# Kernel tuning notes

Measured on AMD Instinct MI355X. Metric: run time of the kernel, lower is better.

Reference implementation:

```python
import jax, jax.numpy as jnp
import numpy as np

PAD_LEFT, PAD_RIGHT = 2, 3


def setup_inputs() -> dict:
    key = jax.random.key(0)
    ks = jax.random.split(key, 7)
    B, T, I, H, O = 256, 2048, 32, 64, 16
    s_ih = 1.0 / np.sqrt(H)
    return {
        "x": jax.random.normal(ks[0], (B, T, I), dtype=jnp.float32),
        "W_ih": jax.random.uniform(ks[1], (H, I), jnp.float32, -s_ih, s_ih),
        "W_hh": jax.random.uniform(ks[2], (H, H), jnp.float32, -s_ih, s_ih),
        "b_ih": jax.random.uniform(ks[3], (H,), jnp.float32, -s_ih, s_ih),
        "b_hh": jax.random.uniform(ks[4], (H,), jnp.float32, -s_ih, s_ih),
        "W_fc": jax.random.uniform(ks[5], (O, H), jnp.float32, -s_ih, s_ih),
        "b_fc": jax.random.uniform(ks[6], (O,), jnp.float32, -s_ih, s_ih),
    }


def reference(x, W_ih, W_hh, b_ih, b_hh, W_fc, b_fc):
    # x: (B, T, I). Zero-pad time axis (ZeroPad1d on permuted tensor).
    B, T, I = x.shape
    H = W_ih.shape[0]
    x_p = jnp.pad(x, ((0, 0), (PAD_LEFT, PAD_RIGHT), (0, 0)))  # (B, Tp, I)
    Tp = T + PAD_LEFT + PAD_RIGHT

    # Precompute input projections for all steps: (Tp, B, H)
    xin = jnp.einsum('bti,hi->tbh', x_p, W_ih) + b_ih + b_hh

    def step(carry, xt):
        h, acc = carry
        h_new = jnp.tanh(xt + h @ W_hh.T)
        return (h_new, acc + h_new), None

    h0 = jnp.zeros((B, H), dtype=x.dtype)
    (h_last, h_sum), _ = jax.lax.scan(step, (h0, jnp.zeros((B, H), x.dtype)), xin)

    # Dropout3d is identity in eval mode; mean over padded time, then fc + relu.
    aggregated = h_sum / Tp  # (B, H)
    return jax.nn.relu(aggregated @ W_fc.T + b_fc)
```

## Files before the change

### kernel.cpp

```cpp
#include <hip/hip_runtime.h>

constexpr int kB = 256;
constexpr int kT = 2048;
constexpr int kI = 32;
constexpr int kH = 64;
constexpr int kO = 16;
constexpr int kPadL = 2;
constexpr int kPadR = 3;
constexpr int kTp = kT + kPadL + kPadR;
constexpr int kCT = 64;
constexpr int kNC = kT / kCT;

constexpr float kS = 1.4426950408889634f;

constexpr unsigned kRbufOff  = 0;
constexpr unsigned kXinOff   = 128;
constexpr unsigned kXinBytes = kCT * kH * 4;
constexpr unsigned kAggOff   = kXinOff + 2 * kXinBytes;
constexpr unsigned kSmemBytes = kAggOff + kH * 4;

typedef float    v2f __attribute__((ext_vector_type(2)));
typedef _Float16 v2h __attribute__((ext_vector_type(2)));
typedef unsigned v4u __attribute__((ext_vector_type(4)));

extern __shared__ char smem[];

__device__ __forceinline__ void pk_fma(v2f& d, v2f a, v2f b) {
  asm("v_pk_fma_f32 %0, %1, %2, %0" : "+v"(d) : "v"(a), "v"(b));
}

__device__ __forceinline__ v2h as_h2(unsigned u) {
  return __builtin_bit_cast(v2h, u);
}

__device__ __forceinline__ float dot2(v2h a, v2h b, float c) {
#if __has_builtin(__builtin_amdgcn_fdot2)
  return __builtin_amdgcn_fdot2(a, b, c, false);
#else
  return fmaf((float)a.x, (float)b.x, fmaf((float)a.y, (float)b.y, c));
#endif
}

__device__ __forceinline__ float exp2_fast(float x) {
#if __has_builtin(__builtin_amdgcn_exp2f)
  return __builtin_amdgcn_exp2f(x);
#else
  return exp2f(x);
#endif
}

#define STEP_LDS_MAIN(q0, q1, q2, q3, q4, q5, q6, q7, xn, rv, xaddr)  \
  asm volatile(                                                       \
      "ds_write_b16 %9, %10\n\t"                                      \
      "ds_read_b128 %0, %11 offset:0\n\t"                             \
      "ds_read_b128 %1, %11 offset:16\n\t"                            \
      "ds_read_b128 %2, %11 offset:32\n\t"                            \
      "ds_read_b128 %3, %11 offset:48\n\t"                            \
      "ds_read_b128 %4, %11 offset:64\n\t"                            \
      "ds_read_b128 %5, %11 offset:80\n\t"                            \
      "ds_read_b128 %6, %11 offset:96\n\t"                            \
      "ds_read_b128 %7, %11 offset:112\n\t"                           \
      "ds_read_b32 %8, %12\n\t"                                       \
      "s_waitcnt lgkmcnt(0)"                                          \
      : "=v"(q0), "=v"(q1), "=v"(q2), "=v"(q3),                       \
        "=v"(q4), "=v"(q5), "=v"(q6), "=v"(q7), "=v"(xn)              \
      : "v"(raddr), "v"(rv), "v"(rbase), "v"(xaddr))

#define STEP_LDS_NOX(q0, q1, q2, q3, q4, q5, q6, q7, rv)              \
  asm volatile(                                                       \
      "ds_write_b16 %8, %9\n\t"                                       \
      "ds_read_b128 %0, %10 offset:0\n\t"                             \
      "ds_read_b128 %1, %10 offset:16\n\t"                            \
      "ds_read_b128 %2, %10 offset:32\n\t"                            \
      "ds_read_b128 %3, %10 offset:48\n\t"                            \
      "ds_read_b128 %4, %10 offset:64\n\t"                            \
      "ds_read_b128 %5, %10 offset:80\n\t"                            \
      "ds_read_b128 %6, %10 offset:96\n\t"                            \
      "ds_read_b128 %7, %10 offset:112\n\t"                           \
      "s_waitcnt lgkmcnt(0)"                                          \
      : "=v"(q0), "=v"(q1), "=v"(q2), "=v"(q3),                       \
        "=v"(q4), "=v"(q5), "=v"(q6), "=v"(q7)                        \
      : "v"(raddr), "v"(rv), "v"(rbase))

__global__ __launch_bounds__(128) void rnn_fused(
    const float* __restrict__ x,
    const float* __restrict__ W_ih,
    const float* __restrict__ W_hh,
    const float* __restrict__ b_ih,
    const float* __restrict__ b_hh,
    const float* __restrict__ W_fc,
    const float* __restrict__ b_fc,
    float* __restrict__ out)
{
  const int b = blockIdx.x;
  const int lane = threadIdx.x & 63;
  const int wave = threadIdx.x >> 6;

  float rowsum = 0.0f;
#pragma unroll
  for (int j = 0; j < kH; j += 4) {
    float4 v = *(const float4*)(W_hh + lane * kH + j);
    rowsum += (v.x + v.y) + (v.z + v.w);
  }
  const float bias2 = 2.0f * kS * (b_ih[lane] + b_hh[lane] + rowsum);

  if (wave == 1) {
    v2f wi2[kI / 2];
#pragma unroll
    for (int i = 0; i < kI; i += 4) {
      float4 v = *(const float4*)(W_ih + lane * kI + i);
      wi2[i / 2 + 0] = v2f{2.0f * kS * v.x, 2.0f * kS * v.y};
      wi2[i / 2 + 1] = v2f{2.0f * kS * v.z, 2.0f * kS * v.w};
    }
    const float* xb = x + (size_t)b * kT * kI;

    auto fill = [&](int c, int buf) {
      const float* src = xb + (size_t)c * kCT * kI;
      float* dst = (float*)(smem + kXinOff + buf * kXinBytes);
#pragma unroll 2
      for (int t = 0; t < kCT; ++t) {
        const float4* row = (const float4*)(src + t * kI);
        v2f a0 = v2f{0.0f, 0.0f}, a1 = v2f{0.0f, 0.0f};
#pragma unroll
        for (int i2 = 0; i2 < 8; ++i2) {
          float4 v = row[i2];
          pk_fma(a0, wi2[2 * i2 + 0], v2f{v.x, v.y});
          pk_fma(a1, wi2[2 * i2 + 1], v2f{v.z, v.w});
        }
        dst[t * kH + lane] = bias2 + ((a0.x + a0.y) + (a1.x + a1.y));
      }
    };

    fill(0, 0);
    __syncthreads();
    for (int c = 0; c < kNC; ++c) {
      if (c + 1 < kNC) fill(c + 1, (c + 1) & 1);
      __syncthreads();
    }
    return;
  }

  v2h wh[kH / 2];
#pragma unroll
  for (int j = 0; j < kH; j += 2) {
    float w0 = W_hh[lane * kH + j + 0];
    float w1 = W_hh[lane * kH + j + 1];
    wh[j / 2] = v2h{(_Float16)(-4.0f * kS * w0), (_Float16)(-4.0f * kS * w1)};
  }

  const unsigned raddr = kRbufOff + (unsigned)lane * 2u;
  unsigned rbase = kRbufOff;

  float rsum = 0.0f;
  unsigned rv = (unsigned)__builtin_bit_cast(unsigned short, (_Float16)0.5f);

  auto tail = [&](const v4u& A, const v4u& B, const v4u& C, const v4u& D,
                  const v4u& E, const v4u& F, const v4u& G, const v4u& H,
                  float za_init) -> float {
    float za = za_init, zb = 0.0f, zc = 0.0f, zd = 0.0f;
    za = dot2(as_h2(A.x), wh[0], za);
    zb = dot2(as_h2(A.y), wh[1], zb);
    zc = dot2(as_h2(A.z), wh[2], zc);
    zd = dot2(as_h2(A.w), wh[3], zd);
    za = dot2(as_h2(B.x), wh[4], za);
    zb = dot2(as_h2(B.y), wh[5], zb);
    zc = dot2(as_h2(B.z), wh[6], zc);
    zd = dot2(as_h2(B.w), wh[7], zd);
    za = dot2(as_h2(C.x), wh[8], za);
    zb = dot2(as_h2(C.y), wh[9], zb);
    zc = dot2(as_h2(C.z), wh[10], zc);
    zd = dot2(as_h2(C.w), wh[11], zd);
    za = dot2(as_h2(D.x), wh[12], za);
    zb = dot2(as_h2(D.y), wh[13], zb);
    zc = dot2(as_h2(D.z), wh[14], zc);
    zd = dot2(as_h2(D.w), wh[15], zd);
    za = dot2(as_h2(E.x), wh[16], za);
    zb = dot2(as_h2(E.y), wh[17], zb);
    zc = dot2(as_h2(E.z), wh[18], zc);
    zd = dot2(as_h2(E.w), wh[19], zd);
    za = dot2(as_h2(F.x), wh[20], za);
    zb = dot2(as_h2(F.y), wh[21], zb);
    zc = dot2(as_h2(F.z), wh[22], zc);
    zd = dot2(as_h2(F.w), wh[23], zd);
    za = dot2(as_h2(G.x), wh[24], za);
    zb = dot2(as_h2(G.y), wh[25], zb);
    zc = dot2(as_h2(G.z), wh[26], zc);
    zd = dot2(as_h2(G.w), wh[27], zd);
    za = dot2(as_h2(H.x), wh[28], za);
    zb = dot2(as_h2(H.y), wh[29], zb);
    zc = dot2(as_h2(H.z), wh[30], zc);
    zd = dot2(as_h2(H.w), wh[31], zd);
    float z2 = (za + zb) + (zc + zd);
    float t = exp2_fast(z2);
    return __builtin_amdgcn_rcpf(1.0f + t);
  };

  auto pad_step = [&]() {
    v4u q0, q1, q2, q3, q4, q5, q6, q7;
    STEP_LDS_NOX(q0, q1, q2, q3, q4, q5, q6, q7, rv);
    float r = tail(q0, q1, q2, q3, q4, q5, q6, q7, bias2);
    rsum += r;
    rv = (unsigned)__builtin_bit_cast(unsigned short, (_Float16)r);
  };

  pad_step();
  pad_step();
  __syncthreads();

  for (int c = 0; c < kNC; ++c) {
    const unsigned xbase = kXinOff + (unsigned)(c & 1) * kXinBytes +
                           (unsigned)lane * 4u;
    float xc;
    asm volatile("ds_read_b32 %0, %1\n\ts_waitcnt lgkmcnt(0)"
                 : "=v"(xc) : "v"(xbase));
#pragma unroll 9
    for (int t = 0; t < kCT - 1; ++t) {
      v4u q0, q1, q2, q3, q4, q5, q6, q7;
      float xn;
      const unsigned xaddr = xbase + (unsigned)(t + 1) * (kH * 4u);
      STEP_LDS_MAIN(q0, q1, q2, q3, q4, q5, q6, q7, xn, rv, xaddr);
      float r = tail(q0, q1, q2, q3, q4, q5, q6, q7, xc);
      rsum += r;
      rv = (unsigned)__builtin_bit_cast(unsigned short, (_Float16)r);
      xc = xn;
    }
    {
      v4u q0, q1, q2, q3, q4, q5, q6, q7;
      STEP_LDS_NOX(q0, q1, q2, q3, q4, q5, q6, q7, rv);
      float r = tail(q0, q1, q2, q3, q4, q5, q6, q7, xc);
      rsum += r;
      rv = (unsigned)__builtin_bit_cast(unsigned short, (_Float16)r);
    }
    __syncthreads();
  }

  pad_step();
  pad_step();
  pad_step();

  float* aggbuf = (float*)(smem + kAggOff);
  aggbuf[lane] = 1.0f - 2.0f * rsum * (1.0f / (float)kTp);
  if (lane < kO) {
    float acc = b_fc[lane];
    const float* wf = W_fc + lane * kH;
#pragma unroll
    for (int j = 0; j < kH; ++j)
      acc = fmaf(wf[j], aggbuf[j], acc);
    out[b * kO + lane] = fmaxf(acc, 0.0f);
  }
}

extern "C" void kernel_launch(void* const* d_in, const int* in_sizes, int n_in,
                              void* d_out, int out_size, void* d_ws, size_t ws_size,
                              hipStream_t stream) {
  const float* x    = (const float*)d_in[0];
  const float* W_ih = (const float*)d_in[1];
  const float* W_hh = (const float*)d_in[2];
  const float* b_ih = (const float*)d_in[3];
  const float* b_hh = (const float*)d_in[4];
  const float* W_fc = (const float*)d_in[5];
  const float* b_fc = (const float*)d_in[6];
  float* out = (float*)d_out;

  rnn_fused<<<dim3(kB), dim3(128), kSmemBytes, stream>>>(
      x, W_ih, W_hh, b_ih, b_hh, W_fc, b_fc, out);
}
```

Before: 572.0 us.

## Interleave two batch recurrences per wave to hide LDS latency

```diff
diff --git a/kernel.cpp b/kernel.cpp
--- a/kernel.cpp
+++ b/kernel.cpp
@@ -8,16 +8,18 @@
 constexpr int kPadL = 2;
 constexpr int kPadR = 3;
 constexpr int kTp = kT + kPadL + kPadR;
-constexpr int kCT = 64;
+constexpr int kCT = 32;
 constexpr int kNC = kT / kCT;
 
 constexpr float kS = 1.4426950408889634f;
 
-constexpr unsigned kRbufOff  = 0;
-constexpr unsigned kXinOff   = 128;
+constexpr unsigned kRbufA = 0;
+constexpr unsigned kRbufB = 128;
+constexpr unsigned kXinA  = 256;
 constexpr unsigned kXinBytes = kCT * kH * 4;
-constexpr unsigned kAggOff   = kXinOff + 2 * kXinBytes;
-constexpr unsigned kSmemBytes = kAggOff + kH * 4;
+constexpr unsigned kXinB  = kXinA + 2 * kXinBytes;
+constexpr unsigned kAgg   = kXinB + 2 * kXinBytes;
+constexpr unsigned kSmemBytes = kAgg + 2 * kH * 4;
 
 typedef float    v2f __attribute__((ext_vector_type(2)));
 typedef _Float16 v2h __attribute__((ext_vector_type(2)));
@@ -49,38 +51,46 @@
 #endif
 }
 
-#define STEP_LDS_MAIN(q0, q1, q2, q3, q4, q5, q6, q7, xn, rv, xaddr)  \
-  asm volatile(                                                       \
-      "ds_write_b16 %9, %10\n\t"                                      \
-      "ds_read_b128 %0, %11 offset:0\n\t"                             \
-      "ds_read_b128 %1, %11 offset:16\n\t"                            \
-      "ds_read_b128 %2, %11 offset:32\n\t"                            \
-      "ds_read_b128 %3, %11 offset:48\n\t"                            \
-      "ds_read_b128 %4, %11 offset:64\n\t"                            \
-      "ds_read_b128 %5, %11 offset:80\n\t"                            \
-      "ds_read_b128 %6, %11 offset:96\n\t"                            \
-      "ds_read_b128 %7, %11 offset:112\n\t"                           \
-      "ds_read_b32 %8, %12\n\t"                                       \
-      "s_waitcnt lgkmcnt(0)"                                          \
-      : "=v"(q0), "=v"(q1), "=v"(q2), "=v"(q3),                       \
-        "=v"(q4), "=v"(q5), "=v"(q6), "=v"(q7), "=v"(xn)              \
+#define ISSUE10(q0, q1, q2, q3, q4, q5, q6, q7, xn, raddr, rv, rbase, xaddr) \
+  asm volatile(                                                              \
+      "ds_write_b16 %9, %10\n\t"                                             \
+      "ds_read_b128 %0, %11 offset:0\n\t"                                    \
+      "ds_read_b128 %1, %11 offset:16\n\t"                                   \
+      "ds_read_b128 %2, %11 offset:32\n\t"                                   \
+      "ds_read_b128 %3, %11 offset:48\n\t"                                   \
+      "ds_read_b128 %4, %11 offset:64\n\t"                                   \
+      "ds_read_b128 %5, %11 offset:80\n\t"                                   \
+      "ds_read_b128 %6, %11 offset:96\n\t"                                   \
+      "ds_read_b128 %7, %11 offset:112\n\t"                                  \
+      "ds_read_b32 %8, %12"                                                  \
+      : "=v"(q0), "=v"(q1), "=v"(q2), "=v"(q3),                              \
+        "=v"(q4), "=v"(q5), "=v"(q6), "=v"(q7), "=v"(xn)                     \
       : "v"(raddr), "v"(rv), "v"(rbase), "v"(xaddr))
 
-#define STEP_LDS_NOX(q0, q1, q2, q3, q4, q5, q6, q7, rv)              \
-  asm volatile(                                                       \
-      "ds_write_b16 %8, %9\n\t"                                       \
-      "ds_read_b128 %0, %10 offset:0\n\t"                             \
-      "ds_read_b128 %1, %10 offset:16\n\t"                            \
-      "ds_read_b128 %2, %10 offset:32\n\t"                            \
-      "ds_read_b128 %3, %10 offset:48\n\t"                            \
-      "ds_read_b128 %4, %10 offset:64\n\t"                            \
-      "ds_read_b128 %5, %10 offset:80\n\t"                            \
-      "ds_read_b128 %6, %10 offset:96\n\t"                            \
-      "ds_read_b128 %7, %10 offset:112\n\t"                           \
-      "s_waitcnt lgkmcnt(0)"                                          \
-      : "=v"(q0), "=v"(q1), "=v"(q2), "=v"(q3),                       \
-        "=v"(q4), "=v"(q5), "=v"(q6), "=v"(q7)                        \
+#define ISSUE9(q0, q1, q2, q3, q4, q5, q6, q7, raddr, rv, rbase)             \
+  asm volatile(                                                              \
+      "ds_write_b16 %8, %9\n\t"                                              \
+      "ds_read_b128 %0, %10 offset:0\n\t"                                    \
+      "ds_read_b128 %1, %10 offset:16\n\t"                                   \
+      "ds_read_b128 %2, %10 offset:32\n\t"                                   \
+      "ds_read_b128 %3, %10 offset:48\n\t"                                   \
+      "ds_read_b128 %4, %10 offset:64\n\t"                                   \
+      "ds_read_b128 %5, %10 offset:80\n\t"                                   \
+      "ds_read_b128 %6, %10 offset:96\n\t"                                   \
+      "ds_read_b128 %7, %10 offset:112"                                      \
+      : "=v"(q0), "=v"(q1), "=v"(q2), "=v"(q3),                              \
+        "=v"(q4), "=v"(q5), "=v"(q6), "=v"(q7)                               \
       : "v"(raddr), "v"(rv), "v"(rbase))
+
+#define WAIT9(N, q0, q1, q2, q3, q4, q5, q6, q7, xn)                         \
+  asm volatile("s_waitcnt lgkmcnt(" N ")"                                    \
+               : "+v"(q0), "+v"(q1), "+v"(q2), "+v"(q3),                     \
+                 "+v"(q4), "+v"(q5), "+v"(q6), "+v"(q7), "+v"(xn))
+
+#define WAIT8(N, q0, q1, q2, q3, q4, q5, q6, q7)                             \
+  asm volatile("s_waitcnt lgkmcnt(" N ")"                                    \
+               : "+v"(q0), "+v"(q1), "+v"(q2), "+v"(q3),                     \
+                 "+v"(q4), "+v"(q5), "+v"(q6), "+v"(q7))
 
 __global__ __launch_bounds__(128) void rnn_fused(
     const float* __restrict__ x,
@@ -92,7 +102,8 @@
     const float* __restrict__ b_fc,
     float* __restrict__ out)
 {
-  const int b = blockIdx.x;
+  const int b0 = blockIdx.x * 2;
+  const int b1 = b0 + 1;
   const int lane = threadIdx.x & 63;
   const int wave = threadIdx.x >> 6;
 
@@ -112,27 +123,37 @@
       wi2[i / 2 + 0] = v2f{2.0f * kS * v.x, 2.0f * kS * v.y};
       wi2[i / 2 + 1] = v2f{2.0f * kS * v.z, 2.0f * kS * v.w};
     }
-    const float* xb = x + (size_t)b * kT * kI;
+    const float* xbA = x + (size_t)b0 * kT * kI;
+    const float* xbB = x + (size_t)b1 * kT * kI;
 
     auto fill = [&](int c, int buf) {
-      const float* src = xb + (size_t)c * kCT * kI;
-      float* dst = (float*)(smem + kXinOff + buf * kXinBytes);
+      const float* srcA = xbA + (size_t)c * kCT * kI;
+      const float* srcB = xbB + (size_t)c * kCT * kI;
+      float* dstA = (float*)(smem + kXinA + buf * kXinBytes);
+      float* dstB = (float*)(smem + kXinB + buf * kXinBytes);
 #pragma unroll 2
       for (int t = 0; t < kCT; ++t) {
-        const float4* row = (const float4*)(src + t * kI);
-        v2f a0 = v2f{0.0f, 0.0f}, a1 = v2f{0.0f, 0.0f};
+        const float4* rowA = (const float4*)(srcA + t * kI);
+        const float4* rowB = (const float4*)(srcB + t * kI);
+        v2f aA0 = v2f{0.f, 0.f}, aA1 = v2f{0.f, 0.f};
+        v2f aB0 = v2f{0.f, 0.f}, aB1 = v2f{0.f, 0.f};
 #pragma unroll
         for (int i2 = 0; i2 < 8; ++i2) {
-          float4 v = row[i2];
-          pk_fma(a0, wi2[2 * i2 + 0], v2f{v.x, v.y});
-          pk_fma(a1, wi2[2 * i2 + 1], v2f{v.z, v.w});
+          float4 vA = rowA[i2];
+          float4 vB = rowB[i2];
+          pk_fma(aA0, wi2[2 * i2 + 0], v2f{vA.x, vA.y});
+          pk_fma(aA1, wi2[2 * i2 + 1], v2f{vA.z, vA.w});
+          pk_fma(aB0, wi2[2 * i2 + 0], v2f{vB.x, vB.y});
+          pk_fma(aB1, wi2[2 * i2 + 1], v2f{vB.z, vB.w});
         }
-        dst[t * kH + lane] = bias2 + ((a0.x + a0.y) + (a1.x + a1.y));
+        dstA[t * kH + lane] = bias2 + ((aA0.x + aA0.y) + (aA1.x + aA1.y));
+        dstB[t * kH + lane] = bias2 + ((aB0.x + aB0.y) + (aB1.x + aB1.y));
       }
     };
 
     fill(0, 0);
     __syncthreads();
+#pragma unroll 1
     for (int c = 0; c < kNC; ++c) {
       if (c + 1 < kNC) fill(c + 1, (c + 1) & 1);
       __syncthreads();
@@ -148,24 +169,27 @@
     wh[j / 2] = v2h{(_Float16)(-4.0f * kS * w0), (_Float16)(-4.0f * kS * w1)};
   }
 
-  const unsigned raddr = kRbufOff + (unsigned)lane * 2u;
-  unsigned rbase = kRbufOff;
-
-  float rsum = 0.0f;
-  unsigned rv = (unsigned)__builtin_bit_cast(unsigned short, (_Float16)0.5f);
-
-  auto tail = [&](const v4u& A, const v4u& B, const v4u& C, const v4u& D,
-                  const v4u& E, const v4u& F, const v4u& G, const v4u& H,
-                  float za_init) -> float {
-    float za = za_init, zb = 0.0f, zc = 0.0f, zd = 0.0f;
+  const unsigned raddrA = kRbufA + (unsigned)lane * 2u;
+  const unsigned raddrB = kRbufB + (unsigned)lane * 2u;
+  const unsigned rbaseA = kRbufA;
+  const unsigned rbaseB = kRbufB;
+
+  float rsumA = 0.0f, rsumB = 0.0f;
+  unsigned rvA = (unsigned)__builtin_bit_cast(unsigned short, (_Float16)0.5f);
+  unsigned rvB = rvA;
+
+  auto compute = [&](const v4u& A, const v4u& Bq, const v4u& C, const v4u& D,
+                     const v4u& E, const v4u& F, const v4u& G, const v4u& H,
+                     float xin, float& rsum, unsigned& rv) {
+    float za = xin, zb = 0.0f, zc = 0.0f, zd = 0.0f;
     za = dot2(as_h2(A.x), wh[0], za);
     zb = dot2(as_h2(A.y), wh[1], zb);
     zc = dot2(as_h2(A.z), wh[2], zc);
     zd = dot2(as_h2(A.w), wh[3], zd);
-    za = dot2(as_h2(B.x), wh[4], za);
-    zb = dot2(as_h2(B.y), wh[5], zb);
-    zc = dot2(as_h2(B.z), wh[6], zc);
-    zd = dot2(as_h2(B.w), wh[7], zd);
+    za = dot2(as_h2(Bq.x), wh[4], za);
+    zb = dot2(as_h2(Bq.y), wh[5], zb);
+    zc = dot2(as_h2(Bq.z), wh[6], zc);
+    zd = dot2(as_h2(Bq.w), wh[7], zd);
     za = dot2(as_h2(C.x), wh[8], za);
     zb = dot2(as_h2(C.y), wh[9], zb);
     zc = dot2(as_h2(C.z), wh[10], zc);
@@ -192,61 +216,90 @@
     zd = dot2(as_h2(H.w), wh[31], zd);
     float z2 = (za + zb) + (zc + zd);
     float t = exp2_fast(z2);
-    return __builtin_amdgcn_rcpf(1.0f + t);
-  };
-
-  auto pad_step = [&]() {
-    v4u q0, q1, q2, q3, q4, q5, q6, q7;
-    STEP_LDS_NOX(q0, q1, q2, q3, q4, q5, q6, q7, rv);
-    float r = tail(q0, q1, q2, q3, q4, q5, q6, q7, bias2);
+    float r = __builtin_amdgcn_rcpf(1.0f + t);
     rsum += r;
     rv = (unsigned)__builtin_bit_cast(unsigned short, (_Float16)r);
   };
 
-  pad_step();
-  pad_step();
+  v4u qA0, qA1, qA2, qA3, qA4, qA5, qA6, qA7;
+  v4u qB0, qB1, qB2, qB3, qB4, qB5, qB6, qB7;
+  float xnA, xnB;
+
+  ISSUE9(qA0, qA1, qA2, qA3, qA4, qA5, qA6, qA7, raddrA, rvA, rbaseA);
+  ISSUE9(qB0, qB1, qB2, qB3, qB4, qB5, qB6, qB7, raddrB, rvB, rbaseB);
+  WAIT8("9", qA0, qA1, qA2, qA3, qA4, qA5, qA6, qA7);
+  compute(qA0, qA1, qA2, qA3, qA4, qA5, qA6, qA7, bias2, rsumA, rvA);
+  ISSUE9(qA0, qA1, qA2, qA3, qA4, qA5, qA6, qA7, raddrA, rvA, rbaseA);
+  WAIT8("9", qB0, qB1, qB2, qB3, qB4, qB5, qB6, qB7);
+  compute(qB0, qB1, qB2, qB3, qB4, qB5, qB6, qB7, bias2, rsumB, rvB);
+  ISSUE9(qB0, qB1, qB2, qB3, qB4, qB5, qB6, qB7, raddrB, rvB, rbaseB);
+  WAIT8("9", qA0, qA1, qA2, qA3, qA4, qA5, qA6, qA7);
+  compute(qA0, qA1, qA2, qA3, qA4, qA5, qA6, qA7, bias2, rsumA, rvA);
+  WAIT8("0", qB0, qB1, qB2, qB3, qB4, qB5, qB6, qB7);
+  compute(qB0, qB1, qB2, qB3, qB4, qB5, qB6, qB7, bias2, rsumB, rvB);
   __syncthreads();
 
+#pragma unroll 1
   for (int c = 0; c < kNC; ++c) {
-    const unsigned xbase = kXinOff + (unsigned)(c & 1) * kXinBytes +
-                           (unsigned)lane * 4u;
-    float xc;
-    asm volatile("ds_read_b32 %0, %1\n\ts_waitcnt lgkmcnt(0)"
-                 : "=v"(xc) : "v"(xbase));
-#pragma unroll 9
+    const unsigned xbA = kXinA + (unsigned)(c & 1) * kXinBytes +
+                         (unsigned)lane * 4u;
+    const unsigned xbB = kXinB + (unsigned)(c & 1) * kXinBytes +
+                         (unsigned)lane * 4u;
+    ISSUE10(qA0, qA1, qA2, qA3, qA4, qA5, qA6, qA7, xnA,
+            raddrA, rvA, rbaseA, xbA);
+    ISSUE10(qB0, qB1, qB2, qB3, qB4, qB5, qB6, qB7, xnB,
+            raddrB, rvB, rbaseB, xbB);
+#pragma unroll 2
     for (int t = 0; t < kCT - 1; ++t) {
-      v4u q0, q1, q2, q3, q4, q5, q6, q7;
-      float xn;
-      const unsigned xaddr = xbase + (unsigned)(t + 1) * (kH * 4u);
-      STEP_LDS_MAIN(q0, q1, q2, q3, q4, q5, q6, q7, xn, rv, xaddr);
-      float r = tail(q0, q1, q2, q3, q4, q5, q6, q7, xc);
-      rsum += r;
-      rv = (unsigned)__builtin_bit_cast(unsigned short, (_Float16)r);
-      xc = xn;
+      WAIT9("10", qA0, qA1, qA2, qA3, qA4, qA5, qA6, qA7, xnA);
+      compute(qA0, qA1, qA2, qA3, qA4, qA5, qA6, qA7, xnA, rsumA, rvA);
+      ISSUE10(qA0, qA1, qA2, qA3, qA4, qA5, qA6, qA7, xnA,
+              raddrA, rvA, rbaseA, xbA + (unsigned)(t + 1) * (kH * 4u));
+      WAIT9("10", qB0, qB1, qB2, qB3, qB4, qB5, qB6, qB7, xnB);
+      compute(qB0, qB1, qB2, qB3, qB4, qB5, qB6, qB7, xnB, rsumB, rvB);
+      ISSUE10(qB0, qB1, qB2, qB3, qB4, qB5, qB6, qB7, xnB,
+              raddrB, rvB, rbaseB, xbB + (unsigned)(t + 1) * (kH * 4u));
     }
-    {
-      v4u q0, q1, q2, q3, q4, q5, q6, q7;
-      STEP_LDS_NOX(q0, q1, q2, q3, q4, q5, q6, q7, rv);
-      float r = tail(q0, q1, q2, q3, q4, q5, q6, q7, xc);
-      rsum += r;
-      rv = (unsigned)__builtin_bit_cast(unsigned short, (_Float16)r);
+    WAIT9("10", qA0, qA1, qA2, qA3, qA4, qA5, qA6, qA7, xnA);
+    compute(qA0, qA1, qA2, qA3, qA4, qA5, qA6, qA7, xnA, rsumA, rvA);
+    WAIT9("0", qB0, qB1, qB2, qB3, qB4, qB5, qB6, qB7, xnB);
+    compute(qB0, qB1, qB2, qB3, qB4, qB5, qB6, qB7, xnB, rsumB, rvB);
+    __syncthreads();
+  }
+
+  ISSUE9(qA0, qA1, qA2, qA3, qA4, qA5, qA6, qA7, raddrA, rvA, rbaseA);
+  ISSUE9(qB0, qB1, qB2, qB3, qB4, qB5, qB6, qB7, raddrB, rvB, rbaseB);
+  WAIT8("9", qA0, qA1, qA2, qA3, qA4, qA5, qA6, qA7);
+  compute(qA0, qA1, qA2, qA3, qA4, qA5, qA6, qA7, bias2, rsumA, rvA);
+  ISSUE9(qA0, qA1, qA2, qA3, qA4, qA5, qA6, qA7, raddrA, rvA, rbaseA);
+  WAIT8("9", qB0, qB1, qB2, qB3, qB4, qB5, qB6, qB7);
+  compute(qB0, qB1, qB2, qB3, qB4, qB5, qB6, qB7, bias2, rsumB, rvB);
+  ISSUE9(qB0, qB1, qB2, qB3, qB4, qB5, qB6, qB7, raddrB, rvB, rbaseB);
+  WAIT8("9", qA0, qA1, qA2, qA3, qA4, qA5, qA6, qA7);
+  compute(qA0, qA1, qA2, qA3, qA4, qA5, qA6, qA7, bias2, rsumA, rvA);
+  ISSUE9(qA0, qA1, qA2, qA3, qA4, qA5, qA6, qA7, raddrA, rvA, rbaseA);
+  WAIT8("9", qB0, qB1, qB2, qB3, qB4, qB5, qB6, qB7);
+  compute(qB0, qB1, qB2, qB3, qB4, qB5, qB6, qB7, bias2, rsumB, rvB);
+  ISSUE9(qB0, qB1, qB2, qB3, qB4, qB5, qB6, qB7, raddrB, rvB, rbaseB);
+  WAIT8("9", qA0, qA1, qA2, qA3, qA4, qA5, qA6, qA7);
+  compute(qA0, qA1, qA2, qA3, qA4, qA5, qA6, qA7, bias2, rsumA, rvA);
+  WAIT8("0", qB0, qB1, qB2, qB3, qB4, qB5, qB6, qB7);
+  compute(qB0, qB1, qB2, qB3, qB4, qB5, qB6, qB7, bias2, rsumB, rvB);
+
+  float* agg = (float*)(smem + kAgg);
+  agg[lane]      = 1.0f - 2.0f * rsumA * (1.0f / (float)kTp);
+  agg[kH + lane] = 1.0f - 2.0f * rsumB * (1.0f / (float)kTp);
+  if (lane < kO) {
+    float accA = b_fc[lane];
+    float accB = accA;
+    const float* wf = W_fc + lane * kH;
+#pragma unroll
+    for (int j = 0; j < kH; ++j) {
+      accA = fmaf(wf[j], agg[j], accA);
+      accB = fmaf(wf[j], agg[kH + j], accB);
     }
-    __syncthreads();
-  }
-
-  pad_step();
-  pad_step();
-  pad_step();
-
-  float* aggbuf = (float*)(smem + kAggOff);
-  aggbuf[lane] = 1.0f - 2.0f * rsum * (1.0f / (float)kTp);
-  if (lane < kO) {
-    float acc = b_fc[lane];
-    const float* wf = W_fc + lane * kH;
-#pragma unroll
-    for (int j = 0; j < kH; ++j)
-      acc = fmaf(wf[j], aggbuf[j], acc);
-    out[b * kO + lane] = fmaxf(acc, 0.0f);
+    out[b0 * kO + lane] = fmaxf(accA, 0.0f);
+    out[b1 * kO + lane] = fmaxf(accB, 0.0f);
   }
 }
 
@@ -262,6 +315,6 @@
   const float* b_fc = (const float*)d_in[6];
   float* out = (float*)d_out;
 
-  rnn_fused<<<dim3(kB), dim3(128), kSmemBytes, stream>>>(
+  rnn_fused<<<dim3(kB / 2), dim3(128), kSmemBytes, stream>>>(
       x, W_ih, W_hh, b_ih, b_hh, W_fc, b_fc, out);
 }
```

Result: slower. 1.128 ms (+97.1%).
